# Kernel tuning notes

Measured on AMD Instinct MI355X. Metric: run time of the kernel, lower is better.

## Reference

```python
import jax, jax.numpy as jnp
import numpy as np

N_NODES = 50000
N_EDGES = 1600000
D = 128
BN_EPS = 1e-5


def setup_inputs() -> dict:
    key = jax.random.key(0)
    ks = jax.random.split(key, 8)
    inp = {
        'x': jax.random.normal(ks[0], (N_NODES, D), dtype=jnp.float32),
        'edge_index': jax.random.randint(ks[1], (2, N_EDGES), 0, N_NODES, dtype=jnp.int64),
    }
    scale = 1.0 / np.sqrt(D)
    for i, k in zip(range(3), ks[2:5]):
        inp[f'W{i}'] = jax.random.normal(k, (D, D), dtype=jnp.float32) * scale
        inp[f'b{i}'] = jnp.zeros((D,), dtype=jnp.float32)
        inp[f'g{i}'] = jnp.ones((D,), dtype=jnp.float32)
        inp[f'be{i}'] = jnp.zeros((D,), dtype=jnp.float32)
    return inp


def _gcn_conv_improved(h, src, dst, W, b, n_nodes):
    # GCNConv(improved=True): A_hat = A + 2I, sym-normalized by D_hat^{-1/2}
    deg = jnp.zeros((n_nodes,), h.dtype).at[dst].add(1.0) + 2.0  # self-loop weight 2
    dinv = jax.lax.rsqrt(deg)
    norm = dinv[src] * dinv[dst]                       # [E]
    hw = h @ W                                         # [N, d_out]
    msg = hw[src] * norm[:, None]                      # [E, d_out] gather
    agg = jax.ops.segment_sum(msg, dst, num_segments=n_nodes)
    agg = agg + (2.0 / deg)[:, None] * hw              # self-loop contribution
    return agg + b


def _bn_relu(h, gamma, beta):
    # BatchNorm1d in training mode: batch stats over nodes, biased variance
    mean = jnp.mean(h, axis=0)
    var = jnp.mean(jnp.square(h - mean), axis=0)
    y = (h - mean) * jax.lax.rsqrt(var + BN_EPS) * gamma + beta
    return jax.nn.relu(y)


def reference(x, edge_index, W0, b0, g0, be0, W1, b1, g1, be1, W2, b2, g2, be2):
    src, dst = edge_index[0], edge_index[1]
    n = x.shape[0]
    h = x
    params = [(W0, b0, g0, be0), (W1, b1, g1, be1), (W2, b2, g2, be2)]
    for (W, b, g, be) in params:  # fixed small layer loop
        h = _gcn_conv_improved(h, src, dst, W, b, n)
        h = _bn_relu(h, g, be)
    return h
```

## Files before the change

kernel.cpp:

```cpp
#include <hip/hip_runtime.h>
#include <math.h>

#define N_NODES 50000
#define N_EDGES 1600000
#define D 128
#define BN_EPS 1e-5f

#define NSLICE 8
#define SLICE_NODES 6250
#define SUBB 24
#define ROWL (NSLICE * SUBB)
#define NREP 64
#define FILL_BLOCKS 2048
#define GEMM0_BLOCKS ((N_NODES + 63) / 64)
#define GEMM_BLOCKS ((N_NODES + 31) / 32)

typedef __attribute__((ext_vector_type(8))) short short8;
typedef __attribute__((ext_vector_type(8))) unsigned short ushort8v;
typedef __attribute__((ext_vector_type(4))) float f32x4;

__device__ __forceinline__ unsigned short f2bf(float f) {
    unsigned u = __float_as_uint(f);
    u += 0x7FFFu + ((u >> 16) & 1u);
    return (unsigned short)(u >> 16);
}
__device__ __forceinline__ float bf2f(unsigned short u) {
    return __uint_as_float(((unsigned)u) << 16);
}

__device__ __forceinline__ void fill_edge(int d, int e, int lo, int hi,
                                          const int* __restrict__ src,
                                          unsigned int* __restrict__ cnt8,
                                          unsigned short* __restrict__ csr) {
    if (d >= lo && d < hi) {
        int s = src[e];
        int t = s / SLICE_NODES;
        unsigned pos = atomicAdd(&cnt8[(d << 3) + t], 1u);
        if (pos < SUBB) csr[(size_t)d * ROWL + t * SUBB + pos] = (unsigned short)s;
    }
}

__device__ __forceinline__ void fill_body(int blk, const int* __restrict__ src,
                                          const int* __restrict__ dst,
                                          unsigned int* __restrict__ cnt8,
                                          unsigned short* __restrict__ csr) {
    int slice = blk & (NSLICE - 1);
    int b = (blk - GEMM0_BLOCKS) >> 3;
    const int stride = (FILL_BLOCKS >> 3) * 256;
    int lo = slice * SLICE_NODES, hi = lo + SLICE_NODES;
    int e = b * 256 + threadIdx.x;
    for (; e + 3 * stride < N_EDGES; e += 4 * stride) {
        int d0 = dst[e];
        int d1 = dst[e + stride];
        int d2 = dst[e + 2 * stride];
        int d3 = dst[e + 3 * stride];
        fill_edge(d0, e, lo, hi, src, cnt8, csr);
        fill_edge(d1, e + stride, lo, hi, src, cnt8, csr);
        fill_edge(d2, e + 2 * stride, lo, hi, src, cnt8, csr);
        fill_edge(d3, e + 3 * stride, lo, hi, src, cnt8, csr);
    }
    for (; e < N_EDGES; e += stride)
        fill_edge(dst[e], e, lo, hi, src, cnt8, csr);
}

__device__ __forceinline__ void gemm_body(int rowbase, const float* __restrict__ Af32,
                                          const unsigned short* __restrict__ Abf,
                                          const unsigned short* __restrict__ Wt,
                                          const float* __restrict__ sc_sh,
                                          const float* __restrict__ dinv,
                                          int apply_bn,
                                          unsigned short* __restrict__ outbf,
                                          unsigned short* Cs) {
    int tid = threadIdx.x;
    int w = tid >> 6;
    int lane = tid & 63;
    int r = lane & 15, quad = lane >> 4;
    rowbase += w * 16;
    int arow = rowbase + r;
    int arowc = (arow < N_NODES) ? arow : 0;

    f32x4 acc[8] = {};
#pragma unroll
    for (int kc = 0; kc < 128; kc += 32) {
        int ko = kc + quad * 8;
        short8 a;
        if (apply_bn) {
            short8 araw = *(const short8*)&Abf[(size_t)arowc * D + ko];
            const float* sc = &sc_sh[ko];
            const float* sh = &sc_sh[128 + ko];
#pragma unroll
            for (int j = 0; j < 8; j++) {
                float v = bf2f((unsigned short)araw[j]);
                v = fmaxf(fmaf(v, sc[j], sh[j]), 0.f);
                a[j] = (short)f2bf(v);
            }
        } else {
            float4 v0 = *(const float4*)&Af32[(size_t)arowc * D + ko];
            float4 v1 = *(const float4*)&Af32[(size_t)arowc * D + ko + 4];
            a[0] = (short)f2bf(v0.x); a[1] = (short)f2bf(v0.y);
            a[2] = (short)f2bf(v0.z); a[3] = (short)f2bf(v0.w);
            a[4] = (short)f2bf(v1.x); a[5] = (short)f2bf(v1.y);
            a[6] = (short)f2bf(v1.z); a[7] = (short)f2bf(v1.w);
        }
#pragma unroll
        for (int ct = 0; ct < 8; ct++) {
            short8 b = *(const short8*)&Wt[(size_t)(ct * 16 + r) * D + ko];
            acc[ct] = __builtin_amdgcn_mfma_f32_16x16x32_bf16(a, b, acc[ct], 0, 0, 0);
        }
    }
    float dv[4] = {1.f, 1.f, 1.f, 1.f};
    if (dinv) {
        float4 d4 = *(const float4*)&dinv[rowbase + quad * 4];
        dv[0] = d4.x; dv[1] = d4.y; dv[2] = d4.z; dv[3] = d4.w;
    }
#pragma unroll
    for (int ct = 0; ct < 8; ct++)
#pragma unroll
        for (int i = 0; i < 4; i++)
            Cs[w * 2176 + (quad * 4 + i) * 136 + ct * 16 + r] = f2bf(acc[ct][i] * dv[i]);

    int r2 = lane >> 2;
    int seg = lane & 3;
    int orow = rowbase + r2;
    if (orow < N_NODES) {
#pragma unroll
        for (int jj = 0; jj < 4; jj++) {
            *(ushort8v*)&outbf[(size_t)orow * D + seg * 32 + jj * 8] =
                *(const ushort8v*)&Cs[w * 2176 + r2 * 136 + seg * 32 + jj * 8];
        }
    }
}

__global__ __launch_bounds__(256) void fused_fill_gemm0_kernel(const int* __restrict__ src,
                                                               const int* __restrict__ dst,
                                                               unsigned int* __restrict__ cnt8,
                                                               unsigned short* __restrict__ csr,
                                                               const float* __restrict__ x,
                                                               const unsigned short* __restrict__ Wt0,
                                                               unsigned short* __restrict__ hwB) {
    __shared__ unsigned short Cs[4 * 2176];
    if (blockIdx.x < GEMM0_BLOCKS) {
        gemm_body(blockIdx.x * 64, x, nullptr, Wt0, nullptr, nullptr, 0, hwB, Cs);
    } else {
        fill_body(blockIdx.x, src, dst, cnt8, csr);
    }
}

__global__ __launch_bounds__(128) void gemm_mfma_kernel(const unsigned short* __restrict__ Abf,
                                                        const unsigned short* __restrict__ Wt,
                                                        const float* __restrict__ sc_sh,
                                                        const float* __restrict__ dinv,
                                                        unsigned short* __restrict__ outbf) {
    __shared__ unsigned short Cs[2 * 2176];
    gemm_body(blockIdx.x * 32, nullptr, Abf, Wt, sc_sh, dinv, 1, outbf, Cs);
}

__global__ void compute_dinv_kernel(const unsigned int* __restrict__ cnt8, float* __restrict__ dinv) {
    int n = blockIdx.x * blockDim.x + threadIdx.x;
    if (n < N_NODES) {
        const uint4* c = (const uint4*)&cnt8[n << 3];
        uint4 a = c[0], b = c[1];
        unsigned deg = a.x + a.y + a.z + a.w + b.x + b.y + b.z + b.w;
        dinv[n] = rsqrtf((float)deg + 2.0f);
    }
}

__global__ void prep_weights_kernel(const float* __restrict__ W0, const float* __restrict__ W1,
                                    const float* __restrict__ W2, unsigned short* __restrict__ Wt) {
    const float* W = (blockIdx.x == 0) ? W0 : (blockIdx.x == 1) ? W1 : W2;
    unsigned short* o = Wt + (size_t)blockIdx.x * D * D;
    int t = threadIdx.x;
    int n = t & 127, half = t >> 7;
    __attribute__((aligned(16))) unsigned short buf[64];
    for (int j = 0; j < 64; j++) {
        int k = half * 64 + j;
        buf[j] = f2bf(W[(size_t)k * D + n]);
    }
    for (int j = 0; j < 64; j += 8)
        *(ushort8v*)&o[(size_t)n * D + half * 64 + j] = *(const ushort8v*)&buf[j];
}

__global__ __launch_bounds__(256) void gather_agg_stats_kernel(const unsigned short* __restrict__ hw,
                                                               const unsigned short* __restrict__ csr,
                                                               const unsigned int* __restrict__ cnt8,
                                                               const float* __restrict__ dinv,
                                                               unsigned short* __restrict__ out,
                                                               float* __restrict__ rep,
                                                               int weighted) {
    __shared__ float part[16][256];
    int g16 = threadIdx.x >> 4, lane = threadIdx.x & 15;
    int g = blockIdx.x * 16 + g16;
    const ushort8v* hwv = (const ushort8v*)hw;
    float di = dinv[g];
    ushort8v sv = hwv[(size_t)g * 16 + lane];
    float w0 = weighted ? (2.f * di) : 2.f;
    float acc[8];
#pragma unroll
    for (int k = 0; k < 8; k++) acc[k] = w0 * bf2f((unsigned short)sv[k]);
    const unsigned short* row = csr + (size_t)g * ROWL;
#pragma unroll 1
    for (int t = 0; t < NSLICE; t++) {
        int dt = (int)cnt8[(g << 3) + t];
        if (dt > SUBB) dt = SUBB;
        int sA = 0, sB = 0; float wA = 0.f, wB = 0.f;
        if (lane < dt) {
            sA = (int)row[t * SUBB + lane];
            if (weighted) wA = dinv[sA];
        }
        if (lane + 16 < dt) {
            sB = (int)row[t * SUBB + 16 + lane];
            if (weighted) wB = dinv[sB];
        }
        int d1 = dt < 16 ? dt : 16;
        if (weighted) {
            for (int j = 0; j < d1; j++) {
                int sj = __shfl(sA, j, 16);
                float wj = __shfl(wA, j, 16);
                ushort8v v = hwv[(size_t)sj * 16 + lane];
#pragma unroll
                for (int k = 0; k < 8; k++) acc[k] = fmaf(wj, bf2f((unsigned short)v[k]), acc[k]);
            }
            for (int j = 0; j < dt - 16; j++) {
                int sj = __shfl(sB, j, 16);
                float wj = __shfl(wB, j, 16);
                ushort8v v = hwv[(size_t)sj * 16 + lane];
#pragma unroll
                for (int k = 0; k < 8; k++) acc[k] = fmaf(wj, bf2f((unsigned short)v[k]), acc[k]);
            }
        } else {
            for (int j = 0; j < d1; j++) {
                int sj = __shfl(sA, j, 16);
                ushort8v v = hwv[(size_t)sj * 16 + lane];
#pragma unroll
                for (int k = 0; k < 8; k++) acc[k] += bf2f((unsigned short)v[k]);
            }
            for (int j = 0; j < dt - 16; j++) {
                int sj = __shfl(sB, j, 16);
                ushort8v v = hwv[(size_t)sj * 16 + lane];
#pragma unroll
                for (int k = 0; k < 8; k++) acc[k] += bf2f((unsigned short)v[k]);
            }
        }
    }
    ushort8v o;
#pragma unroll
    for (int k = 0; k < 8; k++) { acc[k] *= di; o[k] = f2bf(acc[k]); }
    ((ushort8v*)out)[(size_t)g * 16 + lane] = o;

    float4 s0 = make_float4(acc[0], acc[1], acc[2], acc[3]);
    float4 s1 = make_float4(acc[4], acc[5], acc[6], acc[7]);
    *(float4*)&part[g16][lane * 8]     = s0;
    *(float4*)&part[g16][lane * 8 + 4] = s1;
    *(float4*)&part[g16][128 + lane * 8] =
        make_float4(s0.x * s0.x, s0.y * s0.y, s0.z * s0.z, s0.w * s0.w);
    *(float4*)&part[g16][128 + lane * 8 + 4] =
        make_float4(s1.x * s1.x, s1.y * s1.y, s1.z * s1.z, s1.w * s1.w);
    __syncthreads();
    int c = threadIdx.x;
    float tot = 0.f;
#pragma unroll
    for (int g2 = 0; g2 < 16; g2++) tot += part[g2][c];
    atomicAdd(&rep[(blockIdx.x & (NREP - 1)) * 256 + c], tot);
}

__global__ void bn_reduce_finalize_kernel(const float* __restrict__ gamma,
                                          const float* __restrict__ beta,
                                          float* __restrict__ rep,
                                          float* __restrict__ sc_sh) {
    int c = threadIdx.x;
    if (c >= 128) return;
    float s = 0.f, q = 0.f;
#pragma unroll 4
    for (int rr = 0; rr < NREP; rr++) {
        s += rep[rr * 256 + c];
        q += rep[rr * 256 + 128 + c];
        rep[rr * 256 + c] = 0.f;
        rep[rr * 256 + 128 + c] = 0.f;
    }
    float inv_n = 1.0f / (float)N_NODES;
    float mean = s * inv_n;
    float var = q * inv_n - mean * mean;
    float inv = rsqrtf(var + BN_EPS);
    float sc = gamma[c] * inv;
    sc_sh[c] = sc;
    sc_sh[128 + c] = beta[c] - mean * sc;
}

__global__ void bn_apply_kernel(const unsigned short* __restrict__ h,
                                const float* __restrict__ sc_sh,
                                float* __restrict__ out) {
    int i = blockIdx.x * blockDim.x + threadIdx.x;
    int stride = gridDim.x * blockDim.x;
    const int total = N_NODES * 32;
    for (; i < total; i += stride) {
        int cg = i & 31;
        ushort4 u = ((const ushort4*)h)[i];
        float4 sc = ((const float4*)sc_sh)[cg];
        float4 sh = ((const float4*)sc_sh)[32 + cg];
        float4 v;
        v.x = fmaxf(fmaf(bf2f(u.x), sc.x, sh.x), 0.f);
        v.y = fmaxf(fmaf(bf2f(u.y), sc.y, sh.y), 0.f);
        v.z = fmaxf(fmaf(bf2f(u.z), sc.z, sh.z), 0.f);
        v.w = fmaxf(fmaf(bf2f(u.w), sc.w, sh.w), 0.f);
        ((float4*)out)[i] = v;
    }
}

extern "C" void kernel_launch(void* const* d_in, const int* in_sizes, int n_in,
                              void* d_out, int out_size, void* d_ws, size_t ws_size,
                              hipStream_t stream) {
    const float* x = (const float*)d_in[0];
    const int* ei = (const int*)d_in[1];
    const int* src = ei;
    const int* dst = ei + N_EDGES;
    const float* Wm[3] = {(const float*)d_in[2], (const float*)d_in[6], (const float*)d_in[10]};
    const float* gm[3] = {(const float*)d_in[4], (const float*)d_in[8], (const float*)d_in[12]};
    const float* bm[3] = {(const float*)d_in[5], (const float*)d_in[9], (const float*)d_in[13]};

    char* p = (char*)d_ws;
    auto carve = [&](size_t bytes) { char* r = p; p += (bytes + 255) & ~(size_t)255; return r; };
    unsigned short* hwB    = (unsigned short*)carve((size_t)N_NODES * D * sizeof(unsigned short));
    unsigned short* aggbf  = (unsigned short*)carve((size_t)N_NODES * D * sizeof(unsigned short));
    unsigned short* Wt     = (unsigned short*)carve((size_t)3 * D * D * sizeof(unsigned short));
    float*          dinv   = (float*)carve((N_NODES + 64) * sizeof(float));
    unsigned int*   cnt8   = (unsigned int*)carve((size_t)(N_NODES * 8 + NREP * 256) * sizeof(unsigned int));
    float*          rep    = (float*)(cnt8 + (size_t)N_NODES * 8);
    unsigned short* csr    = (unsigned short*)carve((size_t)N_NODES * ROWL * sizeof(unsigned short));
    float*          sc_sh  = (float*)carve(256 * sizeof(float));

    hipMemsetAsync(cnt8, 0, (size_t)(N_NODES * 8 + NREP * 256) * sizeof(unsigned int), stream);
    prep_weights_kernel<<<3, 256, 0, stream>>>(Wm[0], Wm[1], Wm[2], Wt);

    fused_fill_gemm0_kernel<<<GEMM0_BLOCKS + FILL_BLOCKS, 256, 0, stream>>>(
        src, dst, cnt8, csr, x, Wt, hwB);
    compute_dinv_kernel<<<(N_NODES + 255) / 256, 256, 0, stream>>>(cnt8, dinv);

    gather_agg_stats_kernel<<<N_NODES / 16, 256, 0, stream>>>(hwB, csr, cnt8, dinv, aggbf, rep, 1);
    bn_reduce_finalize_kernel<<<1, 128, 0, stream>>>(gm[0], bm[0], rep, sc_sh);

    for (int l = 1; l < 3; l++) {
        gemm_mfma_kernel<<<GEMM_BLOCKS, 128, 0, stream>>>(aggbf, Wt + (size_t)l * D * D, sc_sh, dinv, hwB);
        gather_agg_stats_kernel<<<N_NODES / 16, 256, 0, stream>>>(hwB, csr, cnt8, dinv, aggbf, rep, 0);
        bn_reduce_finalize_kernel<<<1, 128, 0, stream>>>(gm[l], bm[l], rep, sc_sh);
    }
    bn_apply_kernel<<<2048, 256, 0, stream>>>(aggbf, sc_sh, (float*)d_out);
}
```

Baseline: 481.6 us.

## Drop destination-slice partitioning in CSR fill; batch atomics per thread

The CSR fill no longer has each of 8 block groups scan every edge and keep only destinations in its node slice. Each edge is now processed once by a single flattened grid, and the fill block count drops. Loads of src/dst and the atomics are grouped four per iteration so more memory and atomic operations are in flight at once. This removes about 8x redundant reads of dst but gives up the per-slice locality of the atomics and CSR writes, which may now scatter across the whole array.

```diff
diff --git a/kernel.cpp b/kernel.cpp
--- a/kernel.cpp
+++ b/kernel.cpp
@@ -11,7 +11,7 @@
 #define SUBB 24
 #define ROWL (NSLICE * SUBB)
 #define NREP 64
-#define FILL_BLOCKS 2048
+#define FILL_BLOCKS 1264
 #define GEMM0_BLOCKS ((N_NODES + 63) / 64)
 #define GEMM_BLOCKS ((N_NODES + 31) / 32)
 
@@ -28,39 +28,41 @@
     return __uint_as_float(((unsigned)u) << 16);
 }
 
-__device__ __forceinline__ void fill_edge(int d, int e, int lo, int hi,
-                                          const int* __restrict__ src,
-                                          unsigned int* __restrict__ cnt8,
-                                          unsigned short* __restrict__ csr) {
-    if (d >= lo && d < hi) {
-        int s = src[e];
-        int t = s / SLICE_NODES;
-        unsigned pos = atomicAdd(&cnt8[(d << 3) + t], 1u);
-        if (pos < SUBB) csr[(size_t)d * ROWL + t * SUBB + pos] = (unsigned short)s;
-    }
+__device__ __forceinline__ void fill_one(int e, const int* __restrict__ src,
+                                         const int* __restrict__ dst,
+                                         unsigned int* __restrict__ cnt8,
+                                         unsigned short* __restrict__ csr) {
+    int d = dst[e];
+    int s = src[e];
+    int t = s / SLICE_NODES;
+    unsigned pos = atomicAdd(&cnt8[(d << 3) + t], 1u);
+    if (pos < SUBB) csr[(size_t)d * ROWL + t * SUBB + pos] = (unsigned short)s;
 }
 
 __device__ __forceinline__ void fill_body(int blk, const int* __restrict__ src,
                                           const int* __restrict__ dst,
                                           unsigned int* __restrict__ cnt8,
                                           unsigned short* __restrict__ csr) {
-    int slice = blk & (NSLICE - 1);
-    int b = (blk - GEMM0_BLOCKS) >> 3;
-    const int stride = (FILL_BLOCKS >> 3) * 256;
-    int lo = slice * SLICE_NODES, hi = lo + SLICE_NODES;
-    int e = b * 256 + threadIdx.x;
+    const int stride = FILL_BLOCKS * 256;
+    int e = (blk - GEMM0_BLOCKS) * 256 + threadIdx.x;
     for (; e + 3 * stride < N_EDGES; e += 4 * stride) {
-        int d0 = dst[e];
-        int d1 = dst[e + stride];
-        int d2 = dst[e + 2 * stride];
-        int d3 = dst[e + 3 * stride];
-        fill_edge(d0, e, lo, hi, src, cnt8, csr);
-        fill_edge(d1, e + stride, lo, hi, src, cnt8, csr);
-        fill_edge(d2, e + 2 * stride, lo, hi, src, cnt8, csr);
-        fill_edge(d3, e + 3 * stride, lo, hi, src, cnt8, csr);
+        int d0 = dst[e];              int s0 = src[e];
+        int d1 = dst[e + stride];     int s1 = src[e + stride];
+        int d2 = dst[e + 2 * stride]; int s2 = src[e + 2 * stride];
+        int d3 = dst[e + 3 * stride]; int s3 = src[e + 3 * stride];
+        int t0 = s0 / SLICE_NODES, t1 = s1 / SLICE_NODES;
+        int t2 = s2 / SLICE_NODES, t3 = s3 / SLICE_NODES;
+        unsigned p0 = atomicAdd(&cnt8[(d0 << 3) + t0], 1u);
+        unsigned p1 = atomicAdd(&cnt8[(d1 << 3) + t1], 1u);
+        unsigned p2 = atomicAdd(&cnt8[(d2 << 3) + t2], 1u);
+        unsigned p3 = atomicAdd(&cnt8[(d3 << 3) + t3], 1u);
+        if (p0 < SUBB) csr[(size_t)d0 * ROWL + t0 * SUBB + p0] = (unsigned short)s0;
+        if (p1 < SUBB) csr[(size_t)d1 * ROWL + t1 * SUBB + p1] = (unsigned short)s1;
+        if (p2 < SUBB) csr[(size_t)d2 * ROWL + t2 * SUBB + p2] = (unsigned short)s2;
+        if (p3 < SUBB) csr[(size_t)d3 * ROWL + t3 * SUBB + p3] = (unsigned short)s3;
     }
     for (; e < N_EDGES; e += stride)
-        fill_edge(dst[e], e, lo, hi, src, cnt8, csr);
+        fill_one(e, src, dst, cnt8, csr);
 }
 
 __device__ __forceinline__ void gemm_body(int rowbase, const float* __restrict__ Af32,
```

Result: slower. 523.8 us (+8.8%).

## Pre-bin edges by destination slice before CSR fill

Applied to the files above, without the earlier changes.

Adds an edge binning pass that groups edges by destination slice into per-slice global lists, staging them through shared-memory buffers. Each packed entry holds dst in the high 16 bits and src in the low 16 bits. The fill blocks then read only their own slice's list instead of each scanning all edges and discarding seven eighths of them. This cuts the redundant reading of dst and src across slices, and FILL_BLOCKS drops accordingly. In exchange it adds a separate kernel launch and an extra global write and read of the lists. It also packs node ids into 16 bits, but ids run up to 49999, which is above 32767 and still fits in an unsigned 16-bit field.

```diff
diff --git a/kernel.cpp b/kernel.cpp
--- a/kernel.cpp
+++ b/kernel.cpp
@@ -11,7 +11,11 @@
 #define SUBB 24
 #define ROWL (NSLICE * SUBB)
 #define NREP 64
-#define FILL_BLOCKS 2048
+#define LIST_CAP 204800
+#define BIN_TILE 2048
+#define BIN_CAP 512
+#define BIN_BLOCKS ((N_EDGES + BIN_TILE - 1) / BIN_TILE)
+#define FILL_BLOCKS 1264
 #define GEMM0_BLOCKS ((N_NODES + 63) / 64)
 #define GEMM_BLOCKS ((N_NODES + 31) / 32)
 
@@ -28,39 +32,85 @@
     return __uint_as_float(((unsigned)u) << 16);
 }
 
-__device__ __forceinline__ void fill_edge(int d, int e, int lo, int hi,
-                                          const int* __restrict__ src,
-                                          unsigned int* __restrict__ cnt8,
-                                          unsigned short* __restrict__ csr) {
-    if (d >= lo && d < hi) {
-        int s = src[e];
-        int t = s / SLICE_NODES;
-        unsigned pos = atomicAdd(&cnt8[(d << 3) + t], 1u);
-        if (pos < SUBB) csr[(size_t)d * ROWL + t * SUBB + pos] = (unsigned short)s;
-    }
-}
-
-__device__ __forceinline__ void fill_body(int blk, const int* __restrict__ src,
-                                          const int* __restrict__ dst,
+__global__ __launch_bounds__(256) void edge_bin_kernel(const int* __restrict__ src,
+                                                       const int* __restrict__ dst,
+                                                       unsigned int* __restrict__ gcnt,
+                                                       unsigned int* __restrict__ glist) {
+    __shared__ unsigned int lcnt[NSLICE];
+    __shared__ unsigned int lbase[NSLICE];
+    __shared__ unsigned int lbuf[NSLICE * BIN_CAP];
+    int tid = threadIdx.x;
+    if (tid < NSLICE) lcnt[tid] = 0;
+    __syncthreads();
+    int e0 = blockIdx.x * BIN_TILE;
+#pragma unroll
+    for (int j = 0; j < BIN_TILE / 256; j++) {
+        int e = e0 + j * 256 + tid;
+        if (e < N_EDGES) {
+            int d = dst[e];
+            int s = src[e];
+            int sl = d / SLICE_NODES;
+            unsigned val = ((unsigned)d << 16) | (unsigned)s;
+            unsigned pos = atomicAdd(&lcnt[sl], 1u);
+            if (pos < BIN_CAP) {
+                lbuf[sl * BIN_CAP + pos] = val;
+            } else {
+                unsigned gp = atomicAdd(&gcnt[sl], 1u);
+                if (gp < LIST_CAP) glist[(size_t)sl * LIST_CAP + gp] = val;
+            }
+        }
+    }
+    __syncthreads();
+    if (tid < NSLICE) {
+        unsigned c = lcnt[tid];
+        if (c > BIN_CAP) c = BIN_CAP;
+        lcnt[tid] = c;
+        lbase[tid] = atomicAdd(&gcnt[tid], c);
+    }
+    __syncthreads();
+    for (int sl = 0; sl < NSLICE; sl++) {
+        unsigned c = lcnt[sl], b = lbase[sl];
+        for (unsigned j = tid; j < c; j += 256) {
+            unsigned idx = b + j;
+            if (idx < LIST_CAP) glist[(size_t)sl * LIST_CAP + idx] = lbuf[sl * BIN_CAP + j];
+        }
+    }
+}
+
+__device__ __forceinline__ void fill_scatter(unsigned v,
+                                             unsigned int* __restrict__ cnt8,
+                                             unsigned short* __restrict__ csr) {
+    int d = (int)(v >> 16);
+    int s = (int)(v & 0xFFFFu);
+    int t = s / SLICE_NODES;
+    unsigned pos = atomicAdd(&cnt8[(d << 3) + t], 1u);
+    if (pos < SUBB) csr[(size_t)d * ROWL + t * SUBB + pos] = (unsigned short)s;
+}
+
+__device__ __forceinline__ void fill_body(int blk,
+                                          const unsigned int* __restrict__ glist,
+                                          const unsigned int* __restrict__ gcnt,
                                           unsigned int* __restrict__ cnt8,
                                           unsigned short* __restrict__ csr) {
     int slice = blk & (NSLICE - 1);
-    int b = (blk - GEMM0_BLOCKS) >> 3;
+    int trank = (blk - GEMM0_BLOCKS) >> 3;
+    const unsigned int* list = glist + (size_t)slice * LIST_CAP;
+    int L = (int)gcnt[slice];
+    if (L > LIST_CAP) L = LIST_CAP;
     const int stride = (FILL_BLOCKS >> 3) * 256;
-    int lo = slice * SLICE_NODES, hi = lo + SLICE_NODES;
-    int e = b * 256 + threadIdx.x;
-    for (; e + 3 * stride < N_EDGES; e += 4 * stride) {
-        int d0 = dst[e];
-        int d1 = dst[e + stride];
-        int d2 = dst[e + 2 * stride];
-        int d3 = dst[e + 3 * stride];
-        fill_edge(d0, e, lo, hi, src, cnt8, csr);
-        fill_edge(d1, e + stride, lo, hi, src, cnt8, csr);
-        fill_edge(d2, e + 2 * stride, lo, hi, src, cnt8, csr);
-        fill_edge(d3, e + 3 * stride, lo, hi, src, cnt8, csr);
-    }
-    for (; e < N_EDGES; e += stride)
-        fill_edge(dst[e], e, lo, hi, src, cnt8, csr);
+    int k = trank * 256 + threadIdx.x;
+    for (; k + 3 * stride < L; k += 4 * stride) {
+        unsigned v0 = list[k];
+        unsigned v1 = list[k + stride];
+        unsigned v2 = list[k + 2 * stride];
+        unsigned v3 = list[k + 3 * stride];
+        fill_scatter(v0, cnt8, csr);
+        fill_scatter(v1, cnt8, csr);
+        fill_scatter(v2, cnt8, csr);
+        fill_scatter(v3, cnt8, csr);
+    }
+    for (; k < L; k += stride)
+        fill_scatter(list[k], cnt8, csr);
 }
 
 __device__ __forceinline__ void gemm_body(int rowbase, const float* __restrict__ Af32,
@@ -131,8 +181,8 @@
     }
 }
 
-__global__ __launch_bounds__(256) void fused_fill_gemm0_kernel(const int* __restrict__ src,
-                                                               const int* __restrict__ dst,
+__global__ __launch_bounds__(256) void fused_fill_gemm0_kernel(const unsigned int* __restrict__ glist,
+                                                               const unsigned int* __restrict__ gcnt,
                                                                unsigned int* __restrict__ cnt8,
                                                                unsigned short* __restrict__ csr,
                                                                const float* __restrict__ x,
@@ -142,7 +192,7 @@
     if (blockIdx.x < GEMM0_BLOCKS) {
         gemm_body(blockIdx.x * 64, x, nullptr, Wt0, nullptr, nullptr, 0, hwB, Cs);
     } else {
-        fill_body(blockIdx.x, src, dst, cnt8, csr);
+        fill_body(blockIdx.x, glist, gcnt, cnt8, csr);
     }
 }
 
@@ -323,16 +373,20 @@
     unsigned short* aggbf  = (unsigned short*)carve((size_t)N_NODES * D * sizeof(unsigned short));
     unsigned short* Wt     = (unsigned short*)carve((size_t)3 * D * D * sizeof(unsigned short));
     float*          dinv   = (float*)carve((N_NODES + 64) * sizeof(float));
-    unsigned int*   cnt8   = (unsigned int*)carve((size_t)(N_NODES * 8 + NREP * 256) * sizeof(unsigned int));
+    unsigned int*   cnt8   = (unsigned int*)carve((size_t)(N_NODES * 8 + NREP * 256 + 8) * sizeof(unsigned int));
     float*          rep    = (float*)(cnt8 + (size_t)N_NODES * 8);
+    unsigned int*   gcnt   = cnt8 + (size_t)N_NODES * 8 + NREP * 256;
     unsigned short* csr    = (unsigned short*)carve((size_t)N_NODES * ROWL * sizeof(unsigned short));
+    unsigned int*   glist  = (unsigned int*)carve((size_t)NSLICE * LIST_CAP * sizeof(unsigned int));
     float*          sc_sh  = (float*)carve(256 * sizeof(float));
 
-    hipMemsetAsync(cnt8, 0, (size_t)(N_NODES * 8 + NREP * 256) * sizeof(unsigned int), stream);
+    hipMemsetAsync(cnt8, 0, (size_t)(N_NODES * 8 + NREP * 256 + 8) * sizeof(unsigned int), stream);
     prep_weights_kernel<<<3, 256, 0, stream>>>(Wm[0], Wm[1], Wm[2], Wt);
 
+    edge_bin_kernel<<<BIN_BLOCKS, 256, 0, stream>>>(src, dst, gcnt, glist);
+
     fused_fill_gemm0_kernel<<<GEMM0_BLOCKS + FILL_BLOCKS, 256, 0, stream>>>(
-        src, dst, cnt8, csr, x, Wt, hwB);
+        glist, gcnt, cnt8, csr, x, Wt, hwB);
     compute_dinv_kernel<<<(N_NODES + 255) / 256, 256, 0, stream>>>(cnt8, dinv);
 
     gather_agg_stats_kernel<<<N_NODES / 16, 256, 0, stream>>>(hwB, csr, cnt8, dinv, aggbf, rep, 1);
```

Result: slower. 515.7 us (+7.1%).

## Replace global-atomic CSR fill with two-pass range binning and LDS scatter

Applied to the files above, without the earlier changes.

The CSR build no longer scans all edges once per slice with global atomics. It becomes a two-stage pass. First, blocks bin edges by destination range into per-range global segment lists, staging them through LDS buckets. Then one block per 100-node range builds that range's CSR slab and counts in shared memory and writes them out coalesced. This removes the scattered global atomics and writes, and the eight-fold redundant reads of dst, at the cost of an extra kernel launch and an intermediate buffer whose fixed capacity (SEG_CAP) could silently drop edges if a range overflows.

```diff
diff --git a/kernel.cpp b/kernel.cpp
--- a/kernel.cpp
+++ b/kernel.cpp
@@ -11,7 +11,14 @@
 #define SUBB 24
 #define ROWL (NSLICE * SUBB)
 #define NREP 64
-#define FILL_BLOCKS 2048
+
+#define NRANGE 500
+#define RANGE_NODES 100
+#define NSUB 8
+#define SEG_CAP 512
+#define BIN_TILE 2048
+#define BIN_CAP2 16
+#define BIN_BLOCKS ((N_EDGES + BIN_TILE - 1) / BIN_TILE)
 #define GEMM0_BLOCKS ((N_NODES + 63) / 64)
 #define GEMM_BLOCKS ((N_NODES + 31) / 32)
 
@@ -26,41 +33,6 @@
 }
 __device__ __forceinline__ float bf2f(unsigned short u) {
     return __uint_as_float(((unsigned)u) << 16);
-}
-
-__device__ __forceinline__ void fill_edge(int d, int e, int lo, int hi,
-                                          const int* __restrict__ src,
-                                          unsigned int* __restrict__ cnt8,
-                                          unsigned short* __restrict__ csr) {
-    if (d >= lo && d < hi) {
-        int s = src[e];
-        int t = s / SLICE_NODES;
-        unsigned pos = atomicAdd(&cnt8[(d << 3) + t], 1u);
-        if (pos < SUBB) csr[(size_t)d * ROWL + t * SUBB + pos] = (unsigned short)s;
-    }
-}
-
-__device__ __forceinline__ void fill_body(int blk, const int* __restrict__ src,
-                                          const int* __restrict__ dst,
-                                          unsigned int* __restrict__ cnt8,
-                                          unsigned short* __restrict__ csr) {
-    int slice = blk & (NSLICE - 1);
-    int b = (blk - GEMM0_BLOCKS) >> 3;
-    const int stride = (FILL_BLOCKS >> 3) * 256;
-    int lo = slice * SLICE_NODES, hi = lo + SLICE_NODES;
-    int e = b * 256 + threadIdx.x;
-    for (; e + 3 * stride < N_EDGES; e += 4 * stride) {
-        int d0 = dst[e];
-        int d1 = dst[e + stride];
-        int d2 = dst[e + 2 * stride];
-        int d3 = dst[e + 3 * stride];
-        fill_edge(d0, e, lo, hi, src, cnt8, csr);
-        fill_edge(d1, e + stride, lo, hi, src, cnt8, csr);
-        fill_edge(d2, e + 2 * stride, lo, hi, src, cnt8, csr);
-        fill_edge(d3, e + 3 * stride, lo, hi, src, cnt8, csr);
-    }
-    for (; e < N_EDGES; e += stride)
-        fill_edge(dst[e], e, lo, hi, src, cnt8, csr);
 }
 
 __device__ __forceinline__ void gemm_body(int rowbase, const float* __restrict__ Af32,
@@ -131,19 +103,90 @@
     }
 }
 
-__global__ __launch_bounds__(256) void fused_fill_gemm0_kernel(const int* __restrict__ src,
-                                                               const int* __restrict__ dst,
-                                                               unsigned int* __restrict__ cnt8,
-                                                               unsigned short* __restrict__ csr,
-                                                               const float* __restrict__ x,
-                                                               const unsigned short* __restrict__ Wt0,
-                                                               unsigned short* __restrict__ hwB) {
-    __shared__ unsigned short Cs[4 * 2176];
-    if (blockIdx.x < GEMM0_BLOCKS) {
-        gemm_body(blockIdx.x * 64, x, nullptr, Wt0, nullptr, nullptr, 0, hwB, Cs);
+__global__ __launch_bounds__(256) void fused_bin_gemm0_kernel(const int* __restrict__ src,
+                                                              const int* __restrict__ dst,
+                                                              unsigned int* __restrict__ gcnt,
+                                                              unsigned int* __restrict__ glist,
+                                                              const float* __restrict__ x,
+                                                              const unsigned short* __restrict__ Wt0,
+                                                              unsigned short* __restrict__ hwB) {
+    __shared__ __align__(16) char smem[34000];
+    if (blockIdx.x < BIN_BLOCKS) {
+        unsigned* lcnt = (unsigned*)smem;
+        unsigned* lbuf = (unsigned*)(smem + 2000);
+        int tid = threadIdx.x;
+        int sub = blockIdx.x & (NSUB - 1);
+        for (int i = tid; i < NRANGE; i += 256) lcnt[i] = 0;
+        __syncthreads();
+        int e0 = blockIdx.x * BIN_TILE;
+#pragma unroll
+        for (int j = 0; j < BIN_TILE / 256; j++) {
+            int e = e0 + j * 256 + tid;
+            if (e < N_EDGES) {
+                int d = dst[e];
+                int s = src[e];
+                int rg = d / RANGE_NODES;
+                unsigned val = ((unsigned)(d - rg * RANGE_NODES) << 16) | (unsigned)s;
+                unsigned pos = atomicAdd(&lcnt[rg], 1u);
+                if (pos < BIN_CAP2) {
+                    lbuf[rg * BIN_CAP2 + pos] = val;
+                } else {
+                    unsigned gp = atomicAdd(&gcnt[rg * NSUB + sub], 1u);
+                    if (gp < SEG_CAP) glist[(size_t)(rg * NSUB + sub) * SEG_CAP + gp] = val;
+                }
+            }
+        }
+        __syncthreads();
+        for (int rg = tid; rg < NRANGE; rg += 256) {
+            unsigned c = lcnt[rg];
+            if (c > BIN_CAP2) c = BIN_CAP2;
+            if (c == 0) continue;
+            unsigned b = atomicAdd(&gcnt[rg * NSUB + sub], c);
+            unsigned base = (unsigned)(rg * NSUB + sub) * SEG_CAP;
+            for (unsigned j = 0; j < c; j++) {
+                unsigned idx = b + j;
+                if (idx < SEG_CAP) glist[base + idx] = lbuf[rg * BIN_CAP2 + j];
+            }
+        }
     } else {
-        fill_body(blockIdx.x, src, dst, cnt8, csr);
-    }
+        gemm_body((blockIdx.x - BIN_BLOCKS) * 64, x, nullptr, Wt0, nullptr, nullptr, 0, hwB,
+                  (unsigned short*)smem);
+    }
+}
+
+__global__ __launch_bounds__(256) void csr_scatter_kernel(const unsigned int* __restrict__ glist,
+                                                          const unsigned int* __restrict__ gcnt,
+                                                          unsigned int* __restrict__ cnt8,
+                                                          unsigned short* __restrict__ csr) {
+    __shared__ __align__(16) unsigned int cnt[RANGE_NODES * 8];
+    __shared__ __align__(16) unsigned short slab[RANGE_NODES * ROWL];
+    int tid = threadIdx.x;
+    int rg = blockIdx.x;
+    for (int i = tid; i < RANGE_NODES * 8; i += 256) cnt[i] = 0;
+    __syncthreads();
+#pragma unroll 1
+    for (int sub = 0; sub < NSUB; sub++) {
+        unsigned c = gcnt[rg * NSUB + sub];
+        if (c > SEG_CAP) c = SEG_CAP;
+        const unsigned int* seg = glist + (size_t)(rg * NSUB + sub) * SEG_CAP;
+        for (unsigned j = tid; j < c; j += 256) {
+            unsigned v = seg[j];
+            int dl = (int)(v >> 16);
+            int s = (int)(v & 0xFFFFu);
+            int t = s / SLICE_NODES;
+            unsigned pos = atomicAdd(&cnt[dl * 8 + t], 1u);
+            if (pos < SUBB) slab[dl * ROWL + t * SUBB + pos] = (unsigned short)s;
+        }
+    }
+    __syncthreads();
+    unsigned short* crow = csr + (size_t)rg * RANGE_NODES * ROWL;
+    const ushort8v* sl = (const ushort8v*)slab;
+    for (int i = tid; i < RANGE_NODES * ROWL / 8; i += 256)
+        ((ushort8v*)crow)[i] = sl[i];
+    unsigned int* gout = cnt8 + (size_t)rg * RANGE_NODES * 8;
+    const uint4* cl = (const uint4*)cnt;
+    for (int i = tid; i < RANGE_NODES * 8 / 4; i += 256)
+        ((uint4*)gout)[i] = cl[i];
 }
 
 __global__ __launch_bounds__(128) void gemm_mfma_kernel(const unsigned short* __restrict__ Abf,
@@ -323,16 +366,20 @@
     unsigned short* aggbf  = (unsigned short*)carve((size_t)N_NODES * D * sizeof(unsigned short));
     unsigned short* Wt     = (unsigned short*)carve((size_t)3 * D * D * sizeof(unsigned short));
     float*          dinv   = (float*)carve((N_NODES + 64) * sizeof(float));
-    unsigned int*   cnt8   = (unsigned int*)carve((size_t)(N_NODES * 8 + NREP * 256) * sizeof(unsigned int));
+    unsigned int*   cnt8   = (unsigned int*)carve((size_t)(N_NODES * 8 + NREP * 256 + NRANGE * NSUB) * sizeof(unsigned int));
     float*          rep    = (float*)(cnt8 + (size_t)N_NODES * 8);
+    unsigned int*   gcnt   = cnt8 + (size_t)N_NODES * 8 + NREP * 256;
     unsigned short* csr    = (unsigned short*)carve((size_t)N_NODES * ROWL * sizeof(unsigned short));
+    unsigned int*   glist  = (unsigned int*)carve((size_t)NRANGE * NSUB * SEG_CAP * sizeof(unsigned int));
     float*          sc_sh  = (float*)carve(256 * sizeof(float));
 
-    hipMemsetAsync(cnt8, 0, (size_t)(N_NODES * 8 + NREP * 256) * sizeof(unsigned int), stream);
+    hipMemsetAsync(rep, 0, (size_t)(NREP * 256 + NRANGE * NSUB) * sizeof(unsigned int), stream);
     prep_weights_kernel<<<3, 256, 0, stream>>>(Wm[0], Wm[1], Wm[2], Wt);
 
-    fused_fill_gemm0_kernel<<<GEMM0_BLOCKS + FILL_BLOCKS, 256, 0, stream>>>(
-        src, dst, cnt8, csr, x, Wt, hwB);
+    fused_bin_gemm0_kernel<<<BIN_BLOCKS + GEMM0_BLOCKS, 256, 0, stream>>>(
+        src, dst, gcnt, glist, x, Wt, hwB);
+
+    csr_scatter_kernel<<<NRANGE, 256, 0, stream>>>(glist, gcnt, cnt8, csr);
     compute_dinv_kernel<<<(N_NODES + 255) / 256, 256, 0, stream>>>(cnt8, dinv);
 
     gather_agg_stats_kernel<<<N_NODES / 16, 256, 0, stream>>>(hwB, csr, cnt8, dinv, aggbf, rep, 1);
```

Measured after the change: 455.3 us. 1.06x faster.
